# Performance work log

Hardware: AMD Instinct MI355X
Metric: run time of the kernel (lower is better)

The kernel has to match this reference:

```python
import jax, jax.numpy as jnp
import numpy as np

D = 1024      # feature_dim
H = 16        # heads
HD = D // H   # head_dim
B, N = 8, 1024
LN_EPS = 1e-5


def setup_inputs() -> dict:
    key = jax.random.key(0)
    ks = jax.random.split(key, 12)
    s = 0.02
    return {
        "x": jax.random.normal(ks[0], (B, N, D), jnp.float32),
        "Wq": jax.random.normal(ks[1], (D, D), jnp.float32) * s,
        "bq": jnp.zeros((D,), jnp.float32),
        "Wk": jax.random.normal(ks[2], (D, D), jnp.float32) * s,
        "bk": jnp.zeros((D,), jnp.float32),
        "Wv": jax.random.normal(ks[3], (D, D), jnp.float32) * s,
        "bv": jnp.zeros((D,), jnp.float32),
        "pair_bias": jnp.zeros((D, D), jnp.float32),  # init zeros as in torch
        "Wo": jax.random.normal(ks[4], (D, D), jnp.float32) * s,
        "bo": jnp.zeros((D,), jnp.float32),
        "gamma": jnp.ones((D,), jnp.float32),
        "beta": jnp.zeros((D,), jnp.float32),
    }


def reference(x, Wq, bq, Wk, bk, Wv, bv, pair_bias, Wo, bo, gamma, beta):
    b, n, d = x.shape
    residual = x
    # projections -> [b, h, n, hd]
    def split_heads(t):
        return t.reshape(b, n, H, HD).transpose(0, 2, 1, 3)
    q = split_heads(x @ Wq + bq)
    k = split_heads(x @ Wk + bk)
    v = split_heads(x @ Wv + bv)
    # scores + shared pairwise bias (same bias for every batch/head)
    scores = jnp.einsum('bhqd,bhkd->bhqk', q, k) / jnp.sqrt(jnp.float32(HD))
    scores = scores + pair_bias[:n, :n][None, None, :, :]
    attn = jax.nn.softmax(scores, axis=-1)
    # dropout in eval mode == identity
    out = jnp.einsum('bhqk,bhkd->bhqd', attn, v)
    out = out.transpose(0, 2, 1, 3).reshape(b, n, d)
    out = out @ Wo + bo
    out = residual + out
    # LayerNorm
    mu = jnp.mean(out, axis=-1, keepdims=True)
    var = jnp.var(out, axis=-1, keepdims=True)
    out = (out - mu) * jax.lax.rsqrt(var + LN_EPS) * gamma + beta
    return out, attn
```

## Files before the change

### kernel.cpp

```cpp
#include <hip/hip_runtime.h>
#include <hip/hip_bf16.h>
#include <stdint.h>
#include <stddef.h>

#define DI __device__ __forceinline__

typedef unsigned short u16;
typedef float f32x4 __attribute__((ext_vector_type(4)));
typedef short bf16x8 __attribute__((ext_vector_type(8)));
typedef u16 u16x4 __attribute__((ext_vector_type(4)));

constexpr int Mm = 8192;
constexpr int Dd = 1024;
constexpr float LOG2E = 1.44269504088896f;

DI u16 bf(float f) {
  __hip_bfloat16 h = __float2bfloat16(f);
  return *reinterpret_cast<u16*>(&h);
}

DI float b2f(short s) {
  union { float f; unsigned u; } v;
  v.u = ((unsigned)(unsigned short)s) << 16;
  return v.f;
}

DI f32x4 mfma16(bf16x8 a, bf16x8 b, f32x4 c) {
  return __builtin_amdgcn_mfma_f32_16x16x32_bf16(a, b, c, 0, 0, 0);
}

DI void gload16(const u16* g, u16* l) {
  __builtin_amdgcn_global_load_lds(
      (const __attribute__((address_space(1))) void*)(g),
      (__attribute__((address_space(3))) void*)(l), 16, 0, 0);
}

__global__ __launch_bounds__(256) void k_cvt(const float* __restrict__ x,
                                             u16* __restrict__ o) {
  size_t i = (size_t)blockIdx.x * 256 + threadIdx.x;
  float4 v = *(const float4*)(x + i * 4);
  u16x4 r;
  r.x = bf(v.x); r.y = bf(v.y); r.z = bf(v.z); r.w = bf(v.w);
  *(u16x4*)(o + i * 4) = r;
}

__global__ __launch_bounds__(256) void k_pb(const float* __restrict__ pb,
                                            u16* __restrict__ pbb) {
  size_t i = (size_t)blockIdx.x * 256 + threadIdx.x;
  float4 v = *(const float4*)(pb + i * 4);
  u16x4 r;
  r.x = bf(v.x * LOG2E); r.y = bf(v.y * LOG2E);
  r.z = bf(v.z * LOG2E); r.w = bf(v.w * LOG2E);
  *(u16x4*)(pbb + i * 4) = r;
}

__global__ __launch_bounds__(256) void k_tr4(const float* __restrict__ W0,
                                             const float* __restrict__ W1,
                                             const float* __restrict__ W2,
                                             const float* __restrict__ W3,
                                             u16* __restrict__ T0,
                                             u16* __restrict__ T1,
                                             u16* __restrict__ T2,
                                             u16* __restrict__ T3) {
  __shared__ float t[32][33];
  const float* W;
  u16* T;
  switch (blockIdx.z) {
    case 0: W = W0; T = T0; break;
    case 1: W = W1; T = T1; break;
    case 2: W = W2; T = T2; break;
    default: W = W3; T = T3; break;
  }
  int bx = blockIdx.x * 32;
  int by = blockIdx.y * 32;
  int tx = threadIdx.x, ty = threadIdx.y;
#pragma unroll
  for (int i = 0; i < 4; ++i)
    t[ty + i * 8][tx] = W[(size_t)(bx + ty + i * 8) * 1024 + by + tx];
  __syncthreads();
#pragma unroll
  for (int i = 0; i < 4; ++i)
    T[(size_t)(by + ty + i * 8) * 1024 + bx + tx] = bf(t[tx][ty + i * 8]);
}

template <int MODE>
__global__ __launch_bounds__(256) void k_gemm(const u16* __restrict__ A,
                                              const u16* __restrict__ WT,
                                              const float* __restrict__ bias,
                                              const float* __restrict__ resid,
                                              void* __restrict__ outp) {
  __shared__ __align__(16) u16 smem[2 * 128 * 64];
  u16* As = smem;
  u16* Bs = smem + 128 * 64;
  const int tid = threadIdx.x;
  const int lane = tid & 63;
  const int wave = tid >> 6;
  const int brow = blockIdx.y * 128;
  const int bcol = blockIdx.x * 128;
  const int wr = (wave >> 1) * 64;
  const int wc = (wave & 1) * 64;
  const int l15 = lane & 15, l4 = lane >> 4;

  f32x4 acc[4][4] = {};
  const int crow0 = tid >> 3;
  const int kpos = (tid & 7) * 8;

  for (int t = 0; t < 16; ++t) {
    const int k0 = t * 64;
#pragma unroll
    for (int r = 0; r < 4; ++r) {
      int crow = r * 32 + crow0;
      u16* ldsbase_a = As + ((r * 256 + wave * 64) << 3);
      u16* ldsbase_b = Bs + ((r * 256 + wave * 64) << 3);
      gload16(A + (size_t)(brow + crow) * 1024 + k0 + kpos, ldsbase_a);
      gload16(WT + (size_t)(bcol + crow) * 1024 + k0 + kpos, ldsbase_b);
    }
    __syncthreads();
#pragma unroll
    for (int kk = 0; kk < 2; ++kk) {
      bf16x8 af[4], bg[4];
      const int kb = kk * 32 + l4 * 8;
#pragma unroll
      for (int mt = 0; mt < 4; ++mt)
        af[mt] = *(const bf16x8*)(As + (wr + mt * 16 + l15) * 64 + kb);
#pragma unroll
      for (int nt = 0; nt < 4; ++nt)
        bg[nt] = *(const bf16x8*)(Bs + (wc + nt * 16 + l15) * 64 + kb);
#pragma unroll
      for (int mt = 0; mt < 4; ++mt)
#pragma unroll
        for (int nt = 0; nt < 4; ++nt)
          acc[mt][nt] = mfma16(af[mt], bg[nt], acc[mt][nt]);
    }
    __syncthreads();
  }

  if (MODE == 2) {
#pragma unroll
    for (int nt = 0; nt < 4; ++nt) {
      int dl = wc + nt * 16 + l15;
      float bv = bias[bcol + dl];
#pragma unroll
      for (int mt = 0; mt < 4; ++mt) {
        int s4 = wr + mt * 16 + l4 * 4;
        u16x4 pk;
        pk.x = bf(acc[mt][nt][0] + bv);
        pk.y = bf(acc[mt][nt][1] + bv);
        pk.z = bf(acc[mt][nt][2] + bv);
        pk.w = bf(acc[mt][nt][3] + bv);
        *(u16x4*)(smem + dl * 128 + (s4 ^ ((dl & 7) << 3))) = pk;
      }
    }
    __syncthreads();
    const int bb = brow >> 10;
    const int seq0 = brow & 1023;
    const int chunk = tid & 15;
#pragma unroll
    for (int p = 0; p < 8; ++p) {
      int dl = p * 16 + (tid >> 4);
      bf16x8 v = *(const bf16x8*)(smem + dl * 128 + ((chunk * 8) ^ ((dl & 7) << 3)));
      *(bf16x8*)((u16*)outp + ((size_t)bb * 1024 + bcol + dl) * 1024 + seq0 + chunk * 8) = v;
    }
    return;
  }

#pragma unroll
  for (int nt = 0; nt < 4; ++nt) {
    int gc = bcol + wc + nt * 16 + l15;
    float bv = bias[gc];
#pragma unroll
    for (int mt = 0; mt < 4; ++mt) {
#pragma unroll
      for (int i = 0; i < 4; ++i) {
        int gm = brow + wr + mt * 16 + l4 * 4 + i;
        float v = acc[mt][nt][i] + bv;
        if (MODE == 0) {
          ((u16*)outp)[(size_t)gm * 1024 + gc] = bf(v * (0.125f * LOG2E));
        } else if (MODE == 1) {
          ((u16*)outp)[(size_t)gm * 1024 + gc] = bf(v);
        } else {
          ((float*)outp)[(size_t)gm * 1024 + gc] = v + resid[(size_t)gm * 1024 + gc];
        }
      }
    }
  }
}

__global__ __launch_bounds__(512) void k_attn(const u16* __restrict__ q,
                                              const u16* __restrict__ kk_,
                                              const u16* __restrict__ vt,
                                              const u16* __restrict__ pbb,
                                              float* __restrict__ attn_out,
                                              u16* __restrict__ aout) {
  __shared__ __align__(16) u16 sc[32 * 1024];
  __shared__ __align__(16) u16 kst[128 * 64];
  const int tid = threadIdx.x;
  const int lane = tid & 63;
  const int wave = tid >> 6;
  const int bid = blockIdx.x;
  const int swz = (bid & 7) * 512 + (bid >> 3);
  const int bh = swz >> 5;
  const int q0 = (swz & 31) * 32;
  const int b = bh >> 4, h = bh & 15;
  const int l15 = lane & 15, l4 = lane >> 4;

  bf16x8 qf[2][2];
#pragma unroll
  for (int qs = 0; qs < 2; ++qs) {
    const u16* qp = q + ((size_t)(b * 1024 + q0 + qs * 16 + l15)) * 1024 + h * 64 + l4 * 8;
    qf[qs][0] = *(const bf16x8*)qp;
    qf[qs][1] = *(const bf16x8*)(qp + 32);
  }

  for (int c = 0; c < 8; ++c) {
#pragma unroll
    for (int rr = 0; rr < 2; ++rr) {
      int gru = rr * 512 + tid;
      int row = gru >> 3, g = gru & 7;
      int gsw = g ^ (row & 7);
      gload16(kk_ + (size_t)(b * 1024 + c * 128 + row) * 1024 + h * 64 + gsw * 8,
              kst + ((rr * 512 + wave * 64) << 3));
    }
    __syncthreads();
    const int krow = wave * 16 + l15;
    bf16x8 k0 = *(const bf16x8*)(kst + krow * 64 + (((0 + l4) ^ (krow & 7)) << 3));
    bf16x8 k1 = *(const bf16x8*)(kst + krow * 64 + (((4 + l4) ^ (krow & 7)) << 3));
    const int c4 = c * 128 + wave * 16 + l4 * 4;
#pragma unroll
    for (int qs = 0; qs < 2; ++qs) {
      f32x4 cc = {};
      cc = mfma16(k0, qf[qs][0], cc);
      cc = mfma16(k1, qf[qs][1], cc);
      const int lrow = qs * 16 + l15;
      u16x4 pbv = *(const u16x4*)(pbb + (size_t)(q0 + lrow) * 1024 + c4);
      u16x4 pk;
      pk.x = bf(cc[0] + b2f((short)pbv.x));
      pk.y = bf(cc[1] + b2f((short)pbv.y));
      pk.z = bf(cc[2] + b2f((short)pbv.z));
      pk.w = bf(cc[3] + b2f((short)pbv.w));
      *(u16x4*)(sc + lrow * 1024 + (c4 ^ ((lrow & 7) << 3))) = pk;
    }
    __syncthreads();
  }

  {
#pragma unroll
    for (int rr = 0; rr < 2; ++rr) {
      int gru = rr * 512 + tid;
      int rd = gru >> 4, g = gru & 15;
      int gsw = g ^ (rd & 15);
      gload16(vt + (size_t)(b * 1024 + h * 64 + rd) * 1024 + 0 * 128 + gsw * 8,
              kst + ((rr * 512 + wave * 64) << 3));
    }
  }

  {
    const int r = tid >> 4;
    const int l = tid & 15;
    const int rx = (r & 7) << 3;
    u16* rowp = sc + r * 1024;
    bf16x8 R[8];
#pragma unroll
    for (int g = 0; g < 8; ++g)
      R[g] = *(const bf16x8*)(rowp + ((g * 128 + l * 8) ^ rx));
    float mx = -3e38f;
#pragma unroll
    for (int g = 0; g < 8; ++g)
#pragma unroll
      for (int j = 0; j < 8; ++j) mx = fmaxf(mx, b2f(R[g][j]));
#pragma unroll
    for (int o = 1; o < 16; o <<= 1) mx = fmaxf(mx, __shfl_xor(mx, o));
    float sum = 0.f;
    float e[8][8];
#pragma unroll
    for (int g = 0; g < 8; ++g)
#pragma unroll
      for (int j = 0; j < 8; ++j) {
        float t = exp2f(b2f(R[g][j]) - mx);
        e[g][j] = t;
        sum += t;
      }
#pragma unroll
    for (int o = 1; o < 16; o <<= 1) sum += __shfl_xor(sum, o);
    float inv = 1.f / sum;
#pragma unroll
    for (int g = 0; g < 8; ++g) {
      bf16x8 w;
#pragma unroll
      for (int j = 0; j < 8; ++j) w[j] = (short)bf(e[g][j] * inv);
      *(bf16x8*)(rowp + ((g * 128 + l * 8) ^ rx)) = w;
    }
  }
  __syncthreads();

  f32x4 oacc = {};
  const int qh = wave & 1;
  const int dq = wave >> 1;
  const int prow = qh * 16 + l15;
  const int vrow = dq * 16 + l15;
  for (int c = 0; c < 8; ++c) {
#pragma unroll
    for (int ks = 0; ks < 4; ++ks) {
      const int gc = c * 16 + ks * 4 + l4;
      bf16x8 pf = *(const bf16x8*)(sc + prow * 1024 + ((gc ^ (prow & 7)) << 3));
      bf16x8 vf = *(const bf16x8*)(kst + vrow * 128 + (((ks * 4 + l4) ^ (vrow & 15)) << 3));
      oacc = mfma16(pf, vf, oacc);
    }
    __syncthreads();
    if (c < 7) {
#pragma unroll
      for (int rr = 0; rr < 2; ++rr) {
        int gru = rr * 512 + tid;
        int rd = gru >> 4, g = gru & 15;
        int gsw = g ^ (rd & 15);
        gload16(vt + (size_t)(b * 1024 + h * 64 + rd) * 1024 + (c + 1) * 128 + gsw * 8,
                kst + ((rr * 512 + wave * 64) << 3));
      }
      __syncthreads();
    }
  }

#pragma unroll
  for (int i = 0; i < 4; ++i)
    aout[(size_t)(b * 1024 + q0 + qh * 16 + l4 * 4 + i) * 1024 + h * 64 + dq * 16 + l15] =
        bf(oacc[i]);

#pragma unroll
  for (int it = 0; it < 16; ++it) {
    int idx = it * 512 + tid;
    int row = idx >> 8;
    int col4 = idx & 255;
    int ebase = (col4 * 4) ^ ((row & 7) << 3);
    u16x4 p = *(const u16x4*)(sc + row * 1024 + ebase);
    f32x4 w;
    w[0] = b2f((short)p.x); w[1] = b2f((short)p.y);
    w[2] = b2f((short)p.z); w[3] = b2f((short)p.w);
    __builtin_nontemporal_store(
        w, (f32x4*)(attn_out + ((size_t)bh * 1024 + q0 + row) * 1024 + col4 * 4));
  }
}

__global__ __launch_bounds__(256) void k_ln(const float* __restrict__ y,
                                            const float* __restrict__ g,
                                            const float* __restrict__ be,
                                            float* __restrict__ o) {
  const int lane = threadIdx.x & 63;
  const int wave = threadIdx.x >> 6;
  size_t row = (size_t)blockIdx.x * 4 + wave;
  const float* yr = y + row * 1024;
  float4 v[4];
  float s = 0.f, sq = 0.f;
#pragma unroll
  for (int i = 0; i < 4; ++i) {
    v[i] = *(const float4*)(yr + i * 256 + lane * 4);
    s += v[i].x + v[i].y + v[i].z + v[i].w;
    sq += v[i].x * v[i].x + v[i].y * v[i].y + v[i].z * v[i].z + v[i].w * v[i].w;
  }
#pragma unroll
  for (int off = 1; off < 64; off <<= 1) {
    s += __shfl_xor(s, off);
    sq += __shfl_xor(sq, off);
  }
  float mu = s * (1.f / 1024.f);
  float var = sq * (1.f / 1024.f) - mu * mu;
  float rs = rsqrtf(fmaxf(var, 0.f) + 1e-5f);
  float* orow = o + row * 1024;
#pragma unroll
  for (int i = 0; i < 4; ++i) {
    int c = i * 256 + lane * 4;
    float4 gg = *(const float4*)(g + c);
    float4 bb = *(const float4*)(be + c);
    float4 rr;
    rr.x = (v[i].x - mu) * rs * gg.x + bb.x;
    rr.y = (v[i].y - mu) * rs * gg.y + bb.y;
    rr.z = (v[i].z - mu) * rs * gg.z + bb.z;
    rr.w = (v[i].w - mu) * rs * gg.w + bb.w;
    *(float4*)(orow + c) = rr;
  }
}

extern "C" void kernel_launch(void* const* d_in, const int* in_sizes, int n_in,
                              void* d_out, int out_size, void* d_ws, size_t ws_size,
                              hipStream_t stream) {
  const float* x = (const float*)d_in[0];
  const float* Wq = (const float*)d_in[1];
  const float* bq = (const float*)d_in[2];
  const float* Wk = (const float*)d_in[3];
  const float* bk = (const float*)d_in[4];
  const float* Wv = (const float*)d_in[5];
  const float* bv = (const float*)d_in[6];
  const float* pb = (const float*)d_in[7];
  const float* Wo = (const float*)d_in[8];
  const float* bo = (const float*)d_in[9];
  const float* gamma = (const float*)d_in[10];
  const float* beta = (const float*)d_in[11];

  char* ws = (char*)d_ws;
  u16* xb = (u16*)(ws);
  u16* aows = (u16*)(ws);
  u16* wqT = (u16*)(ws + (16u << 20));
  u16* pbb = (u16*)(ws + (16u << 20));
  u16* wkT = (u16*)(ws + (18u << 20));
  u16* wvT = (u16*)(ws + (20u << 20));
  u16* woT = (u16*)(ws + (22u << 20));
  u16* qws = (u16*)(ws + (24u << 20));
  u16* kws = (u16*)(ws + (40u << 20));
  u16* vtws = (u16*)(ws + (56u << 20));
  float* yws = (float*)(ws + (72u << 20));

  float* out_ln = (float*)d_out;
  float* out_attn = out_ln + (size_t)Mm * Dd;

  k_cvt<<<8192, 256, 0, stream>>>(x, xb);
  k_tr4<<<dim3(32, 32, 4), dim3(32, 8), 0, stream>>>(Wq, Wk, Wv, Wo, wqT, wkT, wvT, woT);
  k_gemm<0><<<dim3(8, 64), 256, 0, stream>>>(xb, wqT, bq, nullptr, qws);
  k_pb<<<1024, 256, 0, stream>>>(pb, pbb);
  k_gemm<1><<<dim3(8, 64), 256, 0, stream>>>(xb, wkT, bk, nullptr, kws);
  k_gemm<2><<<dim3(8, 64), 256, 0, stream>>>(xb, wvT, bv, nullptr, vtws);
  k_attn<<<4096, 512, 0, stream>>>(qws, kws, vtws, pbb, out_attn, aows);
  k_gemm<3><<<dim3(8, 64), 256, 0, stream>>>(aows, woT, bo, x, yws);
  k_ln<<<2048, 256, 0, stream>>>(yws, gamma, beta, out_ln);
}
```

Measured before the change: 356.2 us.

## Double-buffer K and V tiles in attention kernel with async prefetch

The attention kernel now stages K and V in 64-row chunks through a two-slot LDS buffer. The next chunk's global-to-LDS load is issued before computing on the current one, with explicit vmcnt waits and raw s_barriers in place of paired __syncthreads. It also adds a min-blocks hint to launch_bounds and recomputes exp2 in softmax instead of keeping a 64-float array, to cut register pressure. The intent is to hide load latency and reduce barriers per chunk, at the cost of more loop iterations and relying on hand-managed vmcnt counts being correct.

```diff
diff --git a/kernel.cpp b/kernel.cpp
--- a/kernel.cpp
+++ b/kernel.cpp
@@ -186,14 +186,14 @@
   }
 }
 
-__global__ __launch_bounds__(512) void k_attn(const u16* __restrict__ q,
-                                              const u16* __restrict__ kk_,
-                                              const u16* __restrict__ vt,
-                                              const u16* __restrict__ pbb,
-                                              float* __restrict__ attn_out,
-                                              u16* __restrict__ aout) {
+__global__ __launch_bounds__(512, 4) void k_attn(const u16* __restrict__ q,
+                                                 const u16* __restrict__ kk_,
+                                                 const u16* __restrict__ vt,
+                                                 const u16* __restrict__ pbb,
+                                                 float* __restrict__ attn_out,
+                                                 u16* __restrict__ aout) {
   __shared__ __align__(16) u16 sc[32 * 1024];
-  __shared__ __align__(16) u16 kst[128 * 64];
+  __shared__ __align__(16) u16 kst[2][4096];
   const int tid = threadIdx.x;
   const int lane = tid & 63;
   const int wave = tid >> 6;
@@ -203,6 +203,9 @@
   const int q0 = (swz & 31) * 32;
   const int b = bh >> 4, h = bh & 15;
   const int l15 = lane & 15, l4 = lane >> 4;
+  const int srow = tid >> 3;
+  const int sgsw = (tid & 7) ^ (srow & 7);
+  u16* const sdst = &kst[0][0];
 
   bf16x8 qf[2][2];
 #pragma unroll
@@ -212,47 +215,49 @@
     qf[qs][1] = *(const bf16x8*)(qp + 32);
   }
 
-  for (int c = 0; c < 8; ++c) {
-#pragma unroll
-    for (int rr = 0; rr < 2; ++rr) {
-      int gru = rr * 512 + tid;
-      int row = gru >> 3, g = gru & 7;
-      int gsw = g ^ (row & 7);
-      gload16(kk_ + (size_t)(b * 1024 + c * 128 + row) * 1024 + h * 64 + gsw * 8,
-              kst + ((rr * 512 + wave * 64) << 3));
-    }
-    __syncthreads();
-    const int krow = wave * 16 + l15;
-    bf16x8 k0 = *(const bf16x8*)(kst + krow * 64 + (((0 + l4) ^ (krow & 7)) << 3));
-    bf16x8 k1 = *(const bf16x8*)(kst + krow * 64 + (((4 + l4) ^ (krow & 7)) << 3));
-    const int c4 = c * 128 + wave * 16 + l4 * 4;
-#pragma unroll
-    for (int qs = 0; qs < 2; ++qs) {
+  gload16(kk_ + (size_t)(b * 1024 + srow) * 1024 + h * 64 + sgsw * 8,
+          &kst[0][wave * 512]);
+#pragma unroll
+  for (int hc = 0; hc < 16; ++hc) {
+    if (hc < 15) {
+      gload16(kk_ + (size_t)(b * 1024 + (hc + 1) * 64 + srow) * 1024 + h * 64 + sgsw * 8,
+              &kst[(hc + 1) & 1][wave * 512]);
+      asm volatile("s_waitcnt vmcnt(1)" ::: "memory");
+    } else {
+      asm volatile("s_waitcnt vmcnt(0)" ::: "memory");
+    }
+    __builtin_amdgcn_sched_barrier(0);
+    __builtin_amdgcn_s_barrier();
+    __builtin_amdgcn_sched_barrier(0);
+    {
+      const int qg = wave >> 2, kvg = wave & 3;
+      const int krow = kvg * 16 + l15;
+      const u16* kb = &kst[hc & 1][krow * 64];
+      bf16x8 k0 = *(const bf16x8*)(kb + ((l4 ^ (krow & 7)) << 3));
+      bf16x8 k1 = *(const bf16x8*)(kb + (((4 + l4) ^ (krow & 7)) << 3));
       f32x4 cc = {};
-      cc = mfma16(k0, qf[qs][0], cc);
-      cc = mfma16(k1, qf[qs][1], cc);
-      const int lrow = qs * 16 + l15;
-      u16x4 pbv = *(const u16x4*)(pbb + (size_t)(q0 + lrow) * 1024 + c4);
+      cc = mfma16(k0, qf[qg][0], cc);
+      cc = mfma16(k1, qf[qg][1], cc);
+      const int ql = qg * 16 + l15;
+      const int c4 = hc * 64 + kvg * 16 + l4 * 4;
+      u16x4 pbv = *(const u16x4*)(pbb + (size_t)(q0 + ql) * 1024 + c4);
       u16x4 pk;
       pk.x = bf(cc[0] + b2f((short)pbv.x));
       pk.y = bf(cc[1] + b2f((short)pbv.y));
       pk.z = bf(cc[2] + b2f((short)pbv.z));
       pk.w = bf(cc[3] + b2f((short)pbv.w));
-      *(u16x4*)(sc + lrow * 1024 + (c4 ^ ((lrow & 7) << 3))) = pk;
-    }
-    __syncthreads();
-  }
-
-  {
-#pragma unroll
-    for (int rr = 0; rr < 2; ++rr) {
-      int gru = rr * 512 + tid;
-      int rd = gru >> 4, g = gru & 15;
-      int gsw = g ^ (rd & 15);
-      gload16(vt + (size_t)(b * 1024 + h * 64 + rd) * 1024 + 0 * 128 + gsw * 8,
-              kst + ((rr * 512 + wave * 64) << 3));
-    }
-  }
+      *(u16x4*)(sc + ql * 1024 + (c4 ^ ((ql & 7) << 3))) = pk;
+    }
+    if (hc < 15) {
+      __builtin_amdgcn_sched_barrier(0);
+      __builtin_amdgcn_s_barrier();
+      __builtin_amdgcn_sched_barrier(0);
+    }
+  }
+  __syncthreads();
+
+  gload16(vt + (size_t)(b * 1024 + h * 64 + srow) * 1024 + sgsw * 8,
+          &kst[0][wave * 512]);
 
   {
     const int r = tid >> 4;
@@ -271,15 +276,10 @@
 #pragma unroll
     for (int o = 1; o < 16; o <<= 1) mx = fmaxf(mx, __shfl_xor(mx, o));
     float sum = 0.f;
-    float e[8][8];
 #pragma unroll
     for (int g = 0; g < 8; ++g)
 #pragma unroll
-      for (int j = 0; j < 8; ++j) {
-        float t = exp2f(b2f(R[g][j]) - mx);
-        e[g][j] = t;
-        sum += t;
-      }
+      for (int j = 0; j < 8; ++j) sum += exp2f(b2f(R[g][j]) - mx);
 #pragma unroll
     for (int o = 1; o < 16; o <<= 1) sum += __shfl_xor(sum, o);
     float inv = 1.f / sum;
@@ -287,7 +287,8 @@
     for (int g = 0; g < 8; ++g) {
       bf16x8 w;
 #pragma unroll
-      for (int j = 0; j < 8; ++j) w[j] = (short)bf(e[g][j] * inv);
+      for (int j = 0; j < 8; ++j)
+        w[j] = (short)bf(exp2f(b2f(R[g][j]) - mx) * inv);
       *(bf16x8*)(rowp + ((g * 128 + l * 8) ^ rx)) = w;
     }
   }
@@ -298,25 +299,31 @@
   const int dq = wave >> 1;
   const int prow = qh * 16 + l15;
   const int vrow = dq * 16 + l15;
-  for (int c = 0; c < 8; ++c) {
-#pragma unroll
-    for (int ks = 0; ks < 4; ++ks) {
-      const int gc = c * 16 + ks * 4 + l4;
+#pragma unroll
+  for (int hc = 0; hc < 16; ++hc) {
+    if (hc < 15) {
+      gload16(vt + (size_t)(b * 1024 + h * 64 + srow) * 1024 + (hc + 1) * 64 + sgsw * 8,
+              &kst[(hc + 1) & 1][wave * 512]);
+      asm volatile("s_waitcnt vmcnt(1)" ::: "memory");
+    } else {
+      asm volatile("s_waitcnt vmcnt(0)" ::: "memory");
+    }
+    __builtin_amdgcn_sched_barrier(0);
+    __builtin_amdgcn_s_barrier();
+    __builtin_amdgcn_sched_barrier(0);
+    const u16* vb = &kst[hc & 1][vrow * 64];
+#pragma unroll
+    for (int ks = 0; ks < 2; ++ks) {
+      const int g = ks * 4 + l4;
+      bf16x8 vf = *(const bf16x8*)(vb + ((g ^ (vrow & 7)) << 3));
+      const int gc = hc * 8 + g;
       bf16x8 pf = *(const bf16x8*)(sc + prow * 1024 + ((gc ^ (prow & 7)) << 3));
-      bf16x8 vf = *(const bf16x8*)(kst + vrow * 128 + (((ks * 4 + l4) ^ (vrow & 15)) << 3));
       oacc = mfma16(pf, vf, oacc);
     }
-    __syncthreads();
-    if (c < 7) {
-#pragma unroll
-      for (int rr = 0; rr < 2; ++rr) {
-        int gru = rr * 512 + tid;
-        int rd = gru >> 4, g = gru & 15;
-        int gsw = g ^ (rd & 15);
-        gload16(vt + (size_t)(b * 1024 + h * 64 + rd) * 1024 + (c + 1) * 128 + gsw * 8,
-                kst + ((rr * 512 + wave * 64) << 3));
-      }
-      __syncthreads();
+    if (hc < 15) {
+      __builtin_amdgcn_sched_barrier(0);
+      __builtin_amdgcn_s_barrier();
+      __builtin_amdgcn_sched_barrier(0);
     }
   }
 
```

Measured after the change: 428.6 us. 1.2x slower.
